# Kernel tuning notes

Hardware: AMD Instinct MI355X
Metric: run time of the kernel (lower is better)

Reference implementation:

```python
import jax, jax.numpy as jnp
import numpy as np

NUM_DATA, MAX_SEQ_LEN, NUM_INPUTS = 256, 2048, 256
NUM_HIDDEN, NUM_OUTPUTS = 1024, 256

def _xavier(key, shape):
    fan_in, fan_out = shape
    limit = float(np.sqrt(6.0 / (fan_in + fan_out)))
    return jax.random.uniform(key, shape, jnp.float32, -limit, limit)

def setup_inputs() -> dict:
    key = jax.random.key(0)
    ks = jax.random.split(key, 8)
    return {
        "x": jax.random.normal(ks[0], (NUM_DATA, MAX_SEQ_LEN, NUM_INPUTS), jnp.float32),
        "W_in1": _xavier(ks[1], (NUM_INPUTS, NUM_HIDDEN)),
        "b_in1": jnp.zeros((NUM_HIDDEN,), jnp.float32),
        "W_rec1": _xavier(ks[2], (NUM_HIDDEN, NUM_HIDDEN)),
        "W_in2": _xavier(ks[3], (NUM_INPUTS, NUM_HIDDEN)),
        "b_in2": jnp.zeros((NUM_HIDDEN,), jnp.float32),
        "W_rec2": _xavier(ks[4], (NUM_HIDDEN, NUM_HIDDEN)),
        "W_out": _xavier(ks[5], (NUM_HIDDEN, NUM_OUTPUTS)),
        "b_out": jnp.zeros((NUM_OUTPUTS,), jnp.float32),
    }

def reference(x, W_in1, b_in1, W_rec1, W_in2, b_in2, W_rec2, W_out, b_out):
    num_data, max_seq_len, _ = x.shape
    num_hidden = W_in1.shape[1]

    def step_fn(carry, inp):
        z1, z2 = carry                      # each [max_seq_len, num_hidden]
        x_seq, step = inp                   # x_seq: [max_seq_len, num_inputs]
        z12 = z1 + z2
        z1_new = jnp.tanh(x_seq @ W_in1 + z12 @ W_rec1 + b_in1)
        z2_cand = jnp.tanh(x_seq @ W_in2 + z2 @ W_rec2 + b_in2)
        # Layer2 holds previous state on odd steps
        z2_new = jnp.where((step % 2) == 1, z2, z2_cand)
        z_out = jnp.tanh(z1_new @ W_out + b_out)[-1, :]  # [num_outputs]
        return (z1_new, z2_new), z_out

    z0 = jnp.zeros((max_seq_len, num_hidden), x.dtype)
    steps = jnp.arange(num_data)
    _, out = jax.lax.scan(step_fn, (z0, z0), (x, steps))
    return out  # [num_data, num_outputs]
```

## Files before the change

### kernel.cpp

```cpp
#include <hip/hip_runtime.h>
#include <math.h>

#define ND  256
#define SEQ 2048
#define NI  256
#define NH  1024
#define NO  256

#define RB   64
#define RT   1024
#define HPB  16
#define NHP  (NH + 1)

#define XTB  32
#define OTB  8

#define AL(p)    __hip_atomic_load((p), __ATOMIC_RELAXED, __HIP_MEMORY_SCOPE_AGENT)
#define AS(p,v)  __hip_atomic_store((p), (v), __ATOMIC_RELAXED, __HIP_MEMORY_SCOPE_AGENT)

__global__ void xproj(const float* __restrict__ x,
                      const float* __restrict__ Win1, const float* __restrict__ b1,
                      const float* __restrict__ Win2, const float* __restrict__ b2,
                      float* __restrict__ X1, float* __restrict__ X2) {
    const int   layer = blockIdx.z;
    const int   t0    = blockIdx.y * XTB;
    const int   h     = blockIdx.x * 256 + threadIdx.x;
    const float* W = layer ? Win2 : Win1;
    const float* b = layer ? b2   : b1;
    float*       X = layer ? X2   : X1;

    __shared__ float lx[XTB][NI];
    for (int idx = threadIdx.x; idx < XTB * NI; idx += 256) {
        int r = idx >> 8, c = idx & (NI - 1);
        lx[r][c] = x[(size_t)(t0 + r) * SEQ * NI + (size_t)(SEQ - 1) * NI + c];
    }
    __syncthreads();

    float acc[XTB];
    float bias = b[h];
    #pragma unroll
    for (int r = 0; r < XTB; ++r) acc[r] = bias;

    for (int i = 0; i < NI; ++i) {
        float wv = W[i * NH + h];
        #pragma unroll
        for (int r = 0; r < XTB; ++r) acc[r] += lx[r][i] * wv;
    }
    #pragma unroll
    for (int r = 0; r < XTB; ++r) X[(t0 + r) * NH + h] = acc[r];
}

__launch_bounds__(RT, 1)
__global__ void recur(const float* __restrict__ Wr1, const float* __restrict__ Wr2,
                      const float* __restrict__ X1,  const float* __restrict__ X2,
                      float* Z12, float* Z2, float* Z1hist, int* bar) {
    __shared__ float lW1[HPB][NHP];
    __shared__ float lW2[HPB][NHP];
    __shared__ float sz [NH];
    __shared__ float sz2[NH];

    const int tid = threadIdx.x;
    const int h0  = blockIdx.x * HPB;

    for (int idx = tid; idx < HPB * NH; idx += RT) {
        int hw = idx & (HPB - 1);
        int k  = idx >> 4;
        lW1[hw][k] = Wr1[(size_t)k * NH + h0 + hw];
        lW2[hw][k] = Wr2[(size_t)k * NH + h0 + hw];
    }
    __syncthreads();

    const int w = tid >> 6;
    const int l = tid & 63;
    const int h = h0 + w;

    float z2h = 0.0f;
    int   cur = 0;

    int* cnt = bar + 32;
    int* gen = bar + 64;

    for (int t = 0; t < ND; ++t) {
        const bool even = (t & 1) == 0;

        sz[tid] = AL(Z12 + cur * NH + tid);
        if (even) sz2[tid] = AL(Z2 + ((t >> 1) & 1) * NH + tid);
        __syncthreads();

        float xv1 = X1[t * NH + h];
        float r1 = 0.0f, r2 = 0.0f, xv2 = 0.0f;
        #pragma unroll
        for (int j = 0; j < 16; ++j) {
            int k = l + 64 * j;
            r1 += sz[k] * lW1[w][k];
        }
        if (even) {
            xv2 = X2[t * NH + h];
            #pragma unroll
            for (int j = 0; j < 16; ++j) {
                int k = l + 64 * j;
                r2 += sz2[k] * lW2[w][k];
            }
        }
        #pragma unroll
        for (int off = 32; off; off >>= 1) {
            r1 += __shfl_xor(r1, off, 64);
            r2 += __shfl_xor(r2, off, 64);
        }

        if (l == 0) {
            float z1n = tanhf(xv1 + r1);
            if (even) z2h = tanhf(xv2 + r2);
            Z1hist[t * NH + h] = z1n;
            AS(Z12 + (cur ^ 1) * NH + h, z1n + z2h);
            if (even) AS(Z2 + (((t >> 1) & 1) ^ 1) * NH + h, z2h);
        }
        cur ^= 1;

        if (t == ND - 1) break;

        __builtin_amdgcn_s_waitcnt(0);
        __syncthreads();
        if (tid == 0) {
            int g = AL(gen);
            int a = __hip_atomic_fetch_add(cnt, 1, __ATOMIC_RELAXED,
                                           __HIP_MEMORY_SCOPE_AGENT);
            if (a == RB - 1) {
                AS(cnt, 0);
                AS(gen, g + 1);
            } else {
                while (AL(gen) == g) { }
            }
        }
        __syncthreads();
    }
}

__global__ void outproj(const float* __restrict__ Z1hist,
                        const float* __restrict__ Wout,
                        const float* __restrict__ bout,
                        float* __restrict__ out) {
    const int t0 = blockIdx.x * OTB;
    const int o  = threadIdx.x;

    __shared__ float lz[OTB][NH];
    for (int idx = threadIdx.x; idx < OTB * NH; idx += 256) {
        int r = idx >> 10, c = idx & (NH - 1);
        lz[r][c] = Z1hist[(t0 + r) * NH + c];
    }
    __syncthreads();

    float acc[OTB];
    float bias = bout[o];
    #pragma unroll
    for (int r = 0; r < OTB; ++r) acc[r] = bias;

    for (int hh = 0; hh < NH; ++hh) {
        float wv = Wout[hh * NO + o];
        #pragma unroll
        for (int r = 0; r < OTB; ++r) acc[r] += lz[r][hh] * wv;
    }
    #pragma unroll
    for (int r = 0; r < OTB; ++r) out[(t0 + r) * NO + o] = tanhf(acc[r]);
}

extern "C" void kernel_launch(void* const* d_in, const int* in_sizes, int n_in,
                              void* d_out, int out_size, void* d_ws, size_t ws_size,
                              hipStream_t stream) {
    const float* x     = (const float*)d_in[0];
    const float* Win1  = (const float*)d_in[1];
    const float* b1    = (const float*)d_in[2];
    const float* Wr1   = (const float*)d_in[3];
    const float* Win2  = (const float*)d_in[4];
    const float* b2    = (const float*)d_in[5];
    const float* Wr2   = (const float*)d_in[6];
    const float* Wout  = (const float*)d_in[7];
    const float* bout  = (const float*)d_in[8];
    float* out = (float*)d_out;

    float* ws   = (float*)d_ws;
    float* Z12  = ws;
    float* Z2   = Z12 + 2 * NH;
    int*   bar  = (int*)(Z2 + 2 * NH);
    float* Z1h  = (float*)(bar + 128);
    float* X1   = Z1h + ND * NH;
    float* X2   = X1 + ND * NH;

    hipMemsetAsync(Z12, 0, (4 * NH) * sizeof(float) + 128 * sizeof(int), stream);

    dim3 xg(NH / 256, ND / XTB, 2);
    xproj<<<xg, 256, 0, stream>>>(x, Win1, b1, Win2, b2, X1, X2);

    recur<<<RB, RT, 0, stream>>>(Wr1, Wr2, X1, X2, Z12, Z2, Z1h, bar);

    outproj<<<ND / OTB, NO, 0, stream>>>(Z1h, Wout, bout, out);
}
```

Measured before the change: 1.707 ms.

## Replace grid barrier with per-element step-tagged 64-bit flag words

Removes the global atomic counter/generation barrier between recurrence steps. Each hidden-state value is now packed into a 64-bit word whose upper half holds the step number, and consumers spin on their own element until its tag matches. Shared staging buffers are double-buffered so the next step can be written while the current one is read. This avoids the serialized fetch-add and the broadcast spin on one address, at the cost of many per-element spin loads and reliance on 64-bit atomic store ordering.

```diff
diff --git a/kernel.cpp b/kernel.cpp
--- a/kernel.cpp
+++ b/kernel.cpp
@@ -15,8 +15,10 @@
 #define XTB  32
 #define OTB  8
 
-#define AL(p)    __hip_atomic_load((p), __ATOMIC_RELAXED, __HIP_MEMORY_SCOPE_AGENT)
-#define AS(p,v)  __hip_atomic_store((p), (v), __ATOMIC_RELAXED, __HIP_MEMORY_SCOPE_AGENT)
+typedef unsigned long long u64;
+
+#define AL64(p)    __hip_atomic_load((p), __ATOMIC_RELAXED, __HIP_MEMORY_SCOPE_AGENT)
+#define AS64(p,v)  __hip_atomic_store((p), (v), __ATOMIC_RELAXED, __HIP_MEMORY_SCOPE_AGENT)
 
 __global__ void xproj(const float* __restrict__ x,
                       const float* __restrict__ Win1, const float* __restrict__ b1,
@@ -53,11 +55,11 @@
 __launch_bounds__(RT, 1)
 __global__ void recur(const float* __restrict__ Wr1, const float* __restrict__ Wr2,
                       const float* __restrict__ X1,  const float* __restrict__ X2,
-                      float* Z12, float* Z2, float* Z1hist, int* bar) {
+                      u64* Z12, u64* Z2, float* Z1hist) {
     __shared__ float lW1[HPB][NHP];
     __shared__ float lW2[HPB][NHP];
-    __shared__ float sz [NH];
-    __shared__ float sz2[NH];
+    __shared__ float sz [2][NH];
+    __shared__ float sz2[2][NH];
 
     const int tid = threadIdx.x;
     const int h0  = blockIdx.x * HPB;
@@ -75,64 +77,58 @@
     const int h = h0 + w;
 
     float z2h = 0.0f;
-    int   cur = 0;
-
-    int* cnt = bar + 32;
-    int* gen = bar + 64;
 
     for (int t = 0; t < ND; ++t) {
         const bool even = (t & 1) == 0;
+        const int  q    = t >> 1;
 
-        sz[tid] = AL(Z12 + cur * NH + tid);
-        if (even) sz2[tid] = AL(Z2 + ((t >> 1) & 1) * NH + tid);
+        float xv1 = X1[t * NH + h];
+        float xv2 = even ? X2[t * NH + h] : 0.0f;
+
+        const u64* p1 = Z12 + (t & 1) * NH + tid;
+        u64 v1 = AL64(p1);
+        u64 v2 = 0;
+        const u64* p2 = Z2 + (q & 1) * NH + tid;
+        if (even) v2 = AL64(p2);
+        while ((unsigned)(v1 >> 32) != (unsigned)t) v1 = AL64(p1);
+        sz[t & 1][tid] = __uint_as_float((unsigned)v1);
+        if (even) {
+            while ((unsigned)(v2 >> 32) != (unsigned)q) v2 = AL64(p2);
+            sz2[q & 1][tid] = __uint_as_float((unsigned)v2);
+        }
         __syncthreads();
 
-        float xv1 = X1[t * NH + h];
-        float r1 = 0.0f, r2 = 0.0f, xv2 = 0.0f;
+        float r1 = 0.0f, r2 = 0.0f;
         #pragma unroll
         for (int j = 0; j < 16; ++j) {
             int k = l + 64 * j;
-            r1 += sz[k] * lW1[w][k];
+            r1 += sz[t & 1][k] * lW1[w][k];
         }
         if (even) {
-            xv2 = X2[t * NH + h];
             #pragma unroll
             for (int j = 0; j < 16; ++j) {
                 int k = l + 64 * j;
-                r2 += sz2[k] * lW2[w][k];
+                r2 += sz2[q & 1][k] * lW2[w][k];
             }
         }
         #pragma unroll
-        for (int off = 32; off; off >>= 1) {
-            r1 += __shfl_xor(r1, off, 64);
-            r2 += __shfl_xor(r2, off, 64);
+        for (int off = 32; off; off >>= 1) r1 += __shfl_xor(r1, off, 64);
+        if (even) {
+            #pragma unroll
+            for (int off = 32; off; off >>= 1) r2 += __shfl_xor(r2, off, 64);
         }
 
         if (l == 0) {
             float z1n = tanhf(xv1 + r1);
             if (even) z2h = tanhf(xv2 + r2);
             Z1hist[t * NH + h] = z1n;
-            AS(Z12 + (cur ^ 1) * NH + h, z1n + z2h);
-            if (even) AS(Z2 + (((t >> 1) & 1) ^ 1) * NH + h, z2h);
-        }
-        cur ^= 1;
-
-        if (t == ND - 1) break;
-
-        __builtin_amdgcn_s_waitcnt(0);
-        __syncthreads();
-        if (tid == 0) {
-            int g = AL(gen);
-            int a = __hip_atomic_fetch_add(cnt, 1, __ATOMIC_RELAXED,
-                                           __HIP_MEMORY_SCOPE_AGENT);
-            if (a == RB - 1) {
-                AS(cnt, 0);
-                AS(gen, g + 1);
-            } else {
-                while (AL(gen) == g) { }
+            u64 o1 = ((u64)(unsigned)(t + 1) << 32) | (u64)__float_as_uint(z1n + z2h);
+            AS64(Z12 + ((t + 1) & 1) * NH + h, o1);
+            if (even) {
+                u64 o2 = ((u64)(unsigned)(q + 1) << 32) | (u64)__float_as_uint(z2h);
+                AS64(Z2 + ((q + 1) & 1) * NH + h, o2);
             }
         }
-        __syncthreads();
     }
 }
 
@@ -178,20 +174,18 @@
     const float* bout  = (const float*)d_in[8];
     float* out = (float*)d_out;
 
-    float* ws   = (float*)d_ws;
-    float* Z12  = ws;
-    float* Z2   = Z12 + 2 * NH;
-    int*   bar  = (int*)(Z2 + 2 * NH);
-    float* Z1h  = (float*)(bar + 128);
-    float* X1   = Z1h + ND * NH;
-    float* X2   = X1 + ND * NH;
+    u64*   Z12 = (u64*)d_ws;
+    u64*   Z2  = Z12 + 2 * NH;
+    float* Z1h = (float*)(Z2 + 2 * NH);
+    float* X1  = Z1h + ND * NH;
+    float* X2  = X1 + ND * NH;
 
-    hipMemsetAsync(Z12, 0, (4 * NH) * sizeof(float) + 128 * sizeof(int), stream);
+    hipMemsetAsync(Z12, 0, 4 * NH * sizeof(u64), stream);
 
     dim3 xg(NH / 256, ND / XTB, 2);
     xproj<<<xg, 256, 0, stream>>>(x, Win1, b1, Win2, b2, X1, X2);
 
-    recur<<<RB, RT, 0, stream>>>(Wr1, Wr2, X1, X2, Z12, Z2, Z1h, bar);
+    recur<<<RB, RT, 0, stream>>>(Wr1, Wr2, X1, X2, Z12, Z2, Z1h);
 
     outproj<<<ND / OTB, NO, 0, stream>>>(Z1h, Wout, bout, out);
 }
```

New measurement: 1.832 ms. +7.3%, slower.
